# Optimization experiments

Measured on AMD Instinct MI355X. Metric: run time of the kernel, lower is better.

The kernel has to match this reference:

```python
import jax, jax.numpy as jnp
import numpy as np

EPS = 1e-12  # torch F.normalize default eps


def setup_inputs() -> dict:
    key = jax.random.key(0)
    k1, k2, k3, k4 = jax.random.split(key, 4)
    dim, heads, b, h, w = 192, 6, 2, 48, 48
    scale = 1.0 / np.sqrt(dim)
    return {
        "inp": jax.random.normal(k1, (b, dim, h, w), dtype=jnp.float32),
        "wq": jax.random.normal(k2, (dim, dim), dtype=jnp.float32) * scale,
        "wk": jax.random.normal(k3, (dim, dim), dtype=jnp.float32) * scale,
        "wv": jax.random.normal(k4, (dim, dim), dtype=jnp.float32) * scale,
        "temperature": jnp.ones((heads, 1, 1), dtype=jnp.float32),
    }


def _l2norm_lastdim(x):
    # torch F.normalize(x, dim=-1): x / max(||x||_2, eps)
    n = jnp.sqrt(jnp.sum(x * x, axis=-1, keepdims=True))
    return x / jnp.maximum(n, EPS)


def reference(inp, wq, wk, wv, temperature):
    b, c, h, w = inp.shape
    heads = temperature.shape[0]
    ch = c // heads
    n = h * w
    x = inp.reshape(b, c, n)  # 1x1 conv == channel matmul
    q = jnp.einsum("oc,bcn->bon", wq, x).reshape(b, heads, ch, n)
    k = jnp.einsum("oc,bcn->bon", wk, x).reshape(b, heads, ch, n)
    v = jnp.einsum("oc,bcn->bon", wv, x).reshape(b, heads, ch, n)
    q = _l2norm_lastdim(q)
    k = _l2norm_lastdim(k)
    # k^T @ q over channel dim -> [b, heads, n, n]; temperature [heads,1,1] broadcasts
    attn = jnp.einsum("bhcn,bhcm->bhnm", k, q) * temperature
    attn = jax.nn.softmax(attn, axis=-1)
    return attn, v
```

## Files before the change

### kernel.cpp

```cpp
#include <hip/hip_runtime.h>
#include <hip/hip_bf16.h>
#include <cstdint>

#define NSP   2304
#define NT    144
#define ATTN_ELEMS 63700992

typedef __attribute__((ext_vector_type(8))) __bf16 bf16x8;
typedef __attribute__((ext_vector_type(4))) float  float4v;

__device__ __forceinline__ unsigned short f2bf(float f) {
  union { float f; unsigned int u; } v; v.f = f;
  unsigned int u = v.u;
  unsigned int r = u + 0x7FFFu + ((u >> 16) & 1u);
  return (unsigned short)(r >> 16);
}

__global__ __launch_bounds__(256) void prep_pack(
    const float* __restrict__ wq, const float* __restrict__ wk,
    const float* __restrict__ wv, const float* __restrict__ x,
    unsigned short* __restrict__ Wp, unsigned short* __restrict__ Xp)
{
  int t = blockIdx.x * 256 + threadIdx.x;
  int lane = t & 63;
  int g = t >> 6;
  int quad = lane >> 4, col = lane & 15;
  union { int4 v; unsigned short u[8]; } o;
  if (g < 216) {
    int mt = g / 6, kc = g % 6;
    int oo = mt * 16 + col;
    int c0 = kc * 32 + quad * 8;
    const float* w = (oo < 192) ? (wq + (size_t)oo * 192)
                   : (oo < 384) ? (wk + (size_t)(oo - 192) * 192)
                                : (wv + (size_t)(oo - 384) * 192);
#pragma unroll
    for (int jj = 0; jj < 8; ++jj) o.u[jj] = f2bf(w[c0 + jj]);
    ((int4*)Wp)[(size_t)g * 64 + lane] = o.v;
  } else {
    int gx = g - 216;
    int kc = gx % 6;
    int bnt = gx / 6;
    int b = bnt / 144;
    int n = (bnt % 144) * 16 + col;
    int c0 = kc * 32 + quad * 8;
    const float* xp = x + ((size_t)b * 192 + c0) * NSP + n;
#pragma unroll
    for (int jj = 0; jj < 8; ++jj) o.u[jj] = f2bf(xp[(size_t)jj * NSP]);
    ((int4*)Xp)[(size_t)gx * 64 + lane] = o.v;
  }
}

__global__ __launch_bounds__(256) void proj_mfma(
    const bf16x8* __restrict__ Wp, const bf16x8* __restrict__ Xp,
    float* __restrict__ qws, float* __restrict__ kws, float* __restrict__ vout)
{
  int lane = threadIdx.x & 63, w = threadIdx.x >> 6;
  int ng = blockIdx.x * 4 + w;
  int mt = blockIdx.y;
  int b  = blockIdx.z;
  int nt0 = ng * 4;
  float4v acc0 = {0.f,0.f,0.f,0.f};
  float4v acc1 = acc0, acc2 = acc0, acc3 = acc0;
#pragma unroll
  for (int kc = 0; kc < 6; ++kc) {
    bf16x8 a = Wp[(size_t)(mt * 6 + kc) * 64 + lane];
    const bf16x8* xb = Xp + (size_t)((b * 144 + nt0) * 6 + kc) * 64 + lane;
    acc0 = __builtin_amdgcn_mfma_f32_16x16x32_bf16(a, xb[0],    acc0, 0, 0, 0);
    acc1 = __builtin_amdgcn_mfma_f32_16x16x32_bf16(a, xb[384],  acc1, 0, 0, 0);
    acc2 = __builtin_amdgcn_mfma_f32_16x16x32_bf16(a, xb[768],  acc2, 0, 0, 0);
    acc3 = __builtin_amdgcn_mfma_f32_16x16x32_bf16(a, xb[1152], acc3, 0, 0, 0);
  }
  int quad = lane >> 4, col = lane & 15;
  int o0 = mt * 16 + quad * 4;
  float* dst;
  if (mt < 12)      dst = qws + ((size_t)b * 192 + o0) * NSP;
  else if (mt < 24) dst = kws + ((size_t)b * 192 + (o0 - 192)) * NSP;
  else              dst = vout + ((size_t)b * 192 + (o0 - 384)) * NSP;
  float4v acc[4] = {acc0, acc1, acc2, acc3};
#pragma unroll
  for (int tt = 0; tt < 4; ++tt)
#pragma unroll
    for (int r = 0; r < 4; ++r)
      dst[(size_t)r * NSP + (nt0 + tt) * 16 + col] = acc[tt][r];
}

__global__ __launch_bounds__(256) void rownorm(
    const float* __restrict__ qws, const float* __restrict__ kws,
    float* __restrict__ inv)
{
  int r = blockIdx.x;
  const float* src = (r < 384) ? (qws + (size_t)r * NSP)
                               : (kws + (size_t)(r - 384) * NSP);
  float s = 0.f;
#pragma unroll
  for (int i = 0; i < 9; ++i) { float v = src[threadIdx.x + 256 * i]; s += v * v; }
#pragma unroll
  for (int off = 32; off > 0; off >>= 1) s += __shfl_down(s, off);
  __shared__ float ls[4];
  if ((threadIdx.x & 63) == 0) ls[threadIdx.x >> 6] = s;
  __syncthreads();
  if (threadIdx.x == 0) {
    float tot = ls[0] + ls[1] + ls[2] + ls[3];
    inv[r] = 1.0f / fmaxf(sqrtf(tot), 1e-12f);
  }
}

__global__ __launch_bounds__(256) void packqk(
    const float* __restrict__ qws, const float* __restrict__ kws,
    const float* __restrict__ inv, const float* __restrict__ temp,
    unsigned short* __restrict__ Qp, unsigned short* __restrict__ Kp)
{
  int which = blockIdx.z;
  int bh = blockIdx.y;
  int nc = blockIdx.x;
  const float* src = which ? kws : qws;
  const float* ivp = inv + which * 384;
  int b = bh / 6, h = bh % 6;
  float tmul = which ? temp[h] : 1.0f;
  __shared__ float xs[32][65];
  int t = threadIdx.x;
  const float* base = src + ((size_t)b * 192 + h * 32) * NSP + nc * 64;
#pragma unroll
  for (int i = 0; i < 8; ++i) {
    int idx = t + 256 * i;
    int ch = idx >> 6, nl = idx & 63;
    xs[ch][nl] = base[(size_t)ch * NSP + nl] * (ivp[b * 192 + h * 32 + ch] * tmul);
  }
  __syncthreads();
  int jl = t >> 6, lane = t & 63, quad = lane >> 4, col = lane & 15;
  int jt = nc * 4 + jl;
  union { int4 v; unsigned short u[8]; } o;
#pragma unroll
  for (int jj = 0; jj < 8; ++jj) o.u[jj] = f2bf(xs[quad * 8 + jj][jl * 16 + col]);
  int4* dst = (int4*)(which ? Kp : Qp);
  dst[(size_t)(bh * 144 + jt) * 64 + lane] = o.v;
}

__global__ __launch_bounds__(256) void attn_kernel(
    const bf16x8* __restrict__ Qp, const bf16x8* __restrict__ Kp,
    float* __restrict__ out)
{
  int lane = threadIdx.x & 63, w = threadIdx.x >> 6;
  int itile = blockIdx.x;
  int bh = blockIdx.y;
  bf16x8 kf = Kp[((size_t)bh * NT + itile) * 64 + lane];
  const bf16x8* qb = Qp + (size_t)bh * NT * 64 + lane;
  int jt0 = w * 36;
  float l0 = 0.f, l1 = 0.f, l2 = 0.f, l3 = 0.f;
  for (int jt = jt0; jt < jt0 + 36; ++jt) {
    bf16x8 qf = qb[(size_t)jt * 64];
    float4v acc = {0.f,0.f,0.f,0.f};
    acc = __builtin_amdgcn_mfma_f32_16x16x32_bf16(qf, kf, acc, 0, 0, 0);
    l0 += __expf(acc[0]);
    l1 += __expf(acc[1]);
    l2 += __expf(acc[2]);
    l3 += __expf(acc[3]);
  }
  float lsum = (l0 + l1) + (l2 + l3);
  lsum += __shfl_xor(lsum, 16);
  lsum += __shfl_xor(lsum, 32);
  __shared__ float ls[4][16];
  if (lane < 16) ls[w][lane] = lsum;
  __syncthreads();
  int quad = lane >> 4, col = lane & 15;
  float invl = 1.0f / (ls[0][col] + ls[1][col] + ls[2][col] + ls[3][col]);
  float* ob = out + (size_t)bh * NSP * NSP
                  + (size_t)(itile * 16 + col) * NSP + quad * 4;
  for (int jt = jt0; jt < jt0 + 36; ++jt) {
    bf16x8 qf = qb[(size_t)jt * 64];
    float4v acc = {0.f,0.f,0.f,0.f};
    acc = __builtin_amdgcn_mfma_f32_16x16x32_bf16(qf, kf, acc, 0, 0, 0);
    float4 o;
    o.x = __expf(acc[0]) * invl;
    o.y = __expf(acc[1]) * invl;
    o.z = __expf(acc[2]) * invl;
    o.w = __expf(acc[3]) * invl;
    *(float4*)(ob + (size_t)jt * 16) = o;
  }
}

extern "C" void kernel_launch(void* const* d_in, const int* in_sizes, int n_in,
                              void* d_out, int out_size, void* d_ws, size_t ws_size,
                              hipStream_t stream) {
  const float* x    = (const float*)d_in[0];
  const float* wq   = (const float*)d_in[1];
  const float* wk   = (const float*)d_in[2];
  const float* wv   = (const float*)d_in[3];
  const float* temp = (const float*)d_in[4];

  float* attn_out = (float*)d_out;
  float* vout     = attn_out + (size_t)ATTN_ELEMS;

  float* qws = (float*)d_ws;
  float* kws = qws + 884736;
  float* inv = kws + 884736;
  unsigned short* Wp = (unsigned short*)(inv + 768);
  unsigned short* Xp = Wp + 110592;
  unsigned short* Qp = Xp + 884736;
  unsigned short* Kp = Qp + 884736;

  hipLaunchKernelGGL(prep_pack, dim3(486), dim3(256), 0, stream,
                     wq, wk, wv, x, Wp, Xp);
  hipLaunchKernelGGL(proj_mfma, dim3(9, 36, 2), dim3(256), 0, stream,
                     (const bf16x8*)Wp, (const bf16x8*)Xp, qws, kws, vout);
  hipLaunchKernelGGL(rownorm, dim3(768), dim3(256), 0, stream, qws, kws, inv);
  hipLaunchKernelGGL(packqk, dim3(36, 12, 2), dim3(256), 0, stream,
                     qws, kws, inv, temp, Qp, Kp);
  hipLaunchKernelGGL(attn_kernel, dim3(144, 12), dim3(256), 0, stream,
                     (const bf16x8*)Qp, (const bf16x8*)Kp, attn_out);
}
```

Before: 296.9 us.

## Stage softmax exponentials in LDS, fuse row norms into projection, coalesce stores

The attention kernel now writes its first-pass exponentials as bf16 into a padded LDS tile. The normalize-and-store pass reads that tile and writes full contiguous rows with nontemporal float4 stores, instead of recomputing the MFMA and exp and writing 64-byte strided fragments. The separate rownorm kernel is removed: sums of squares are reduced in proj_mfma and accumulated with atomics, and packqk computes the inverse norm itself. V outputs also use nontemporal stores. The change trades about 74 KB of LDS per block (lower occupancy) and bf16 rounding of the exponentials for fewer launches and better-coalesced writes of the dominant output.

```diff
diff --git a/kernel.cpp b/kernel.cpp
--- a/kernel.cpp
+++ b/kernel.cpp
@@ -5,6 +5,8 @@
 #define NSP   2304
 #define NT    144
 #define ATTN_ELEMS 63700992
+#define EPAD  2312
+#define ATTN_LDS (16*EPAD*2 + 64*4 + 16*4)
 
 typedef __attribute__((ext_vector_type(8))) __bf16 bf16x8;
 typedef __attribute__((ext_vector_type(4))) float  float4v;
@@ -19,8 +21,13 @@
 __global__ __launch_bounds__(256) void prep_pack(
     const float* __restrict__ wq, const float* __restrict__ wk,
     const float* __restrict__ wv, const float* __restrict__ x,
-    unsigned short* __restrict__ Wp, unsigned short* __restrict__ Xp)
-{
+    unsigned short* __restrict__ Wp, unsigned short* __restrict__ Xp,
+    float* __restrict__ sumsq)
+{
+  if (blockIdx.x < 3) {
+    int z = blockIdx.x * 256 + threadIdx.x;
+    if (z < 768) sumsq[z] = 0.0f;
+  }
   int t = blockIdx.x * 256 + threadIdx.x;
   int lane = t & 63;
   int g = t >> 6;
@@ -52,7 +59,8 @@
 
 __global__ __launch_bounds__(256) void proj_mfma(
     const bf16x8* __restrict__ Wp, const bf16x8* __restrict__ Xp,
-    float* __restrict__ qws, float* __restrict__ kws, float* __restrict__ vout)
+    float* __restrict__ qws, float* __restrict__ kws, float* __restrict__ vout,
+    float* __restrict__ sumsq)
 {
   int lane = threadIdx.x & 63, w = threadIdx.x >> 6;
   int ng = blockIdx.x * 4 + w;
@@ -72,49 +80,49 @@
   }
   int quad = lane >> 4, col = lane & 15;
   int o0 = mt * 16 + quad * 4;
+  float4v acc[4] = {acc0, acc1, acc2, acc3};
+  bool isv = (mt >= 24);
   float* dst;
   if (mt < 12)      dst = qws + ((size_t)b * 192 + o0) * NSP;
   else if (mt < 24) dst = kws + ((size_t)b * 192 + (o0 - 192)) * NSP;
   else              dst = vout + ((size_t)b * 192 + (o0 - 384)) * NSP;
-  float4v acc[4] = {acc0, acc1, acc2, acc3};
 #pragma unroll
   for (int tt = 0; tt < 4; ++tt)
 #pragma unroll
+    for (int r = 0; r < 4; ++r) {
+      float* p = dst + (size_t)r * NSP + (nt0 + tt) * 16 + col;
+      if (isv) __builtin_nontemporal_store(acc[tt][r], p);
+      else     *p = acc[tt][r];
+    }
+  if (!isv) {
+    float s[4];
+#pragma unroll
     for (int r = 0; r < 4; ++r)
-      dst[(size_t)r * NSP + (nt0 + tt) * 16 + col] = acc[tt][r];
-}
-
-__global__ __launch_bounds__(256) void rownorm(
-    const float* __restrict__ qws, const float* __restrict__ kws,
-    float* __restrict__ inv)
-{
-  int r = blockIdx.x;
-  const float* src = (r < 384) ? (qws + (size_t)r * NSP)
-                               : (kws + (size_t)(r - 384) * NSP);
-  float s = 0.f;
-#pragma unroll
-  for (int i = 0; i < 9; ++i) { float v = src[threadIdx.x + 256 * i]; s += v * v; }
-#pragma unroll
-  for (int off = 32; off > 0; off >>= 1) s += __shfl_down(s, off);
-  __shared__ float ls[4];
-  if ((threadIdx.x & 63) == 0) ls[threadIdx.x >> 6] = s;
-  __syncthreads();
-  if (threadIdx.x == 0) {
-    float tot = ls[0] + ls[1] + ls[2] + ls[3];
-    inv[r] = 1.0f / fmaxf(sqrtf(tot), 1e-12f);
+      s[r] = acc0[r]*acc0[r] + acc1[r]*acc1[r] + acc2[r]*acc2[r] + acc3[r]*acc3[r];
+#pragma unroll
+    for (int off = 1; off < 16; off <<= 1)
+#pragma unroll
+      for (int r = 0; r < 4; ++r) s[r] += __shfl_xor(s[r], off);
+    if (col == 0) {
+      int base = (mt < 12) ? (b * 192 + mt * 16)
+                           : (384 + b * 192 + (mt - 12) * 16);
+#pragma unroll
+      for (int r = 0; r < 4; ++r)
+        atomicAdd(&sumsq[base + quad * 4 + r], s[r]);
+    }
   }
 }
 
 __global__ __launch_bounds__(256) void packqk(
     const float* __restrict__ qws, const float* __restrict__ kws,
-    const float* __restrict__ inv, const float* __restrict__ temp,
+    const float* __restrict__ sumsq, const float* __restrict__ temp,
     unsigned short* __restrict__ Qp, unsigned short* __restrict__ Kp)
 {
   int which = blockIdx.z;
   int bh = blockIdx.y;
   int nc = blockIdx.x;
   const float* src = which ? kws : qws;
-  const float* ivp = inv + which * 384;
+  const float* ssp = sumsq + which * 384;
   int b = bh / 6, h = bh % 6;
   float tmul = which ? temp[h] : 1.0f;
   __shared__ float xs[32][65];
@@ -124,7 +132,9 @@
   for (int i = 0; i < 8; ++i) {
     int idx = t + 256 * i;
     int ch = idx >> 6, nl = idx & 63;
-    xs[ch][nl] = base[(size_t)ch * NSP + nl] * (ivp[b * 192 + h * 32 + ch] * tmul);
+    float ss = ssp[b * 192 + h * 32 + ch];
+    float iv = tmul / fmaxf(sqrtf(ss), 1e-12f);
+    xs[ch][nl] = base[(size_t)ch * NSP + nl] * iv;
   }
   __syncthreads();
   int jl = t >> 6, lane = t & 63, quad = lane >> 4, col = lane & 15;
@@ -140,42 +150,53 @@
     const bf16x8* __restrict__ Qp, const bf16x8* __restrict__ Kp,
     float* __restrict__ out)
 {
-  int lane = threadIdx.x & 63, w = threadIdx.x >> 6;
+  extern __shared__ char smem[];
+  unsigned short* eS = (unsigned short*)smem;
+  float* ls   = (float*)(smem + 16 * EPAD * 2);
+  float* invf = ls + 64;
+  int t = threadIdx.x;
+  int lane = t & 63, w = t >> 6;
   int itile = blockIdx.x;
   int bh = blockIdx.y;
   bf16x8 kf = Kp[((size_t)bh * NT + itile) * 64 + lane];
   const bf16x8* qb = Qp + (size_t)bh * NT * 64 + lane;
+  int quad = lane >> 4, col = lane & 15;
   int jt0 = w * 36;
   float l0 = 0.f, l1 = 0.f, l2 = 0.f, l3 = 0.f;
+  unsigned short* ewp = eS + col * EPAD + quad * 4;
   for (int jt = jt0; jt < jt0 + 36; ++jt) {
     bf16x8 qf = qb[(size_t)jt * 64];
     float4v acc = {0.f,0.f,0.f,0.f};
     acc = __builtin_amdgcn_mfma_f32_16x16x32_bf16(qf, kf, acc, 0, 0, 0);
-    l0 += __expf(acc[0]);
-    l1 += __expf(acc[1]);
-    l2 += __expf(acc[2]);
-    l3 += __expf(acc[3]);
+    float e0 = __expf(acc[0]), e1 = __expf(acc[1]);
+    float e2 = __expf(acc[2]), e3 = __expf(acc[3]);
+    l0 += e0; l1 += e1; l2 += e2; l3 += e3;
+    union { uint2 v; unsigned short u[4]; } pk;
+    pk.u[0] = f2bf(e0); pk.u[1] = f2bf(e1);
+    pk.u[2] = f2bf(e2); pk.u[3] = f2bf(e3);
+    *(uint2*)(ewp + jt * 16) = pk.v;
   }
   float lsum = (l0 + l1) + (l2 + l3);
   lsum += __shfl_xor(lsum, 16);
   lsum += __shfl_xor(lsum, 32);
-  __shared__ float ls[4][16];
-  if (lane < 16) ls[w][lane] = lsum;
+  if (lane < 16) ls[w * 16 + lane] = lsum;
   __syncthreads();
-  int quad = lane >> 4, col = lane & 15;
-  float invl = 1.0f / (ls[0][col] + ls[1][col] + ls[2][col] + ls[3][col]);
-  float* ob = out + (size_t)bh * NSP * NSP
-                  + (size_t)(itile * 16 + col) * NSP + quad * 4;
-  for (int jt = jt0; jt < jt0 + 36; ++jt) {
-    bf16x8 qf = qb[(size_t)jt * 64];
-    float4v acc = {0.f,0.f,0.f,0.f};
-    acc = __builtin_amdgcn_mfma_f32_16x16x32_bf16(qf, kf, acc, 0, 0, 0);
-    float4 o;
-    o.x = __expf(acc[0]) * invl;
-    o.y = __expf(acc[1]) * invl;
-    o.z = __expf(acc[2]) * invl;
-    o.w = __expf(acc[3]) * invl;
-    *(float4*)(ob + (size_t)jt * 16) = o;
+  if (t < 16) invf[t] = 1.0f / (ls[t] + ls[16 + t] + ls[32 + t] + ls[48 + t]);
+  __syncthreads();
+  float* obase = out + (size_t)bh * NSP * NSP + (size_t)(itile * 16) * NSP;
+#pragma unroll 4
+  for (int it = 0; it < 36; ++it) {
+    int c = it * 256 + t;
+    int i = c / 576;
+    int j4 = c - i * 576;
+    float iv = invf[i];
+    uint2 pk = *(const uint2*)(eS + i * EPAD + j4 * 4);
+    float4v o;
+    o.x = __uint_as_float(pk.x << 16) * iv;
+    o.y = __uint_as_float(pk.x & 0xffff0000u) * iv;
+    o.z = __uint_as_float(pk.y << 16) * iv;
+    o.w = __uint_as_float(pk.y & 0xffff0000u) * iv;
+    __builtin_nontemporal_store(o, (float4v*)(obase + (size_t)i * NSP + j4 * 4));
   }
 }
 
@@ -193,19 +214,25 @@
 
   float* qws = (float*)d_ws;
   float* kws = qws + 884736;
-  float* inv = kws + 884736;
-  unsigned short* Wp = (unsigned short*)(inv + 768);
+  float* sumsq = kws + 884736;
+  unsigned short* Wp = (unsigned short*)(sumsq + 768);
   unsigned short* Xp = Wp + 110592;
   unsigned short* Qp = Xp + 884736;
   unsigned short* Kp = Qp + 884736;
 
+  static bool attr_set = false;
+  if (!attr_set) {
+    (void)hipFuncSetAttribute((const void*)attn_kernel,
+                        hipFuncAttributeMaxDynamicSharedMemorySize, ATTN_LDS);
+    attr_set = true;
+  }
+
   hipLaunchKernelGGL(prep_pack, dim3(486), dim3(256), 0, stream,
-                     wq, wk, wv, x, Wp, Xp);
+                     wq, wk, wv, x, Wp, Xp, sumsq);
   hipLaunchKernelGGL(proj_mfma, dim3(9, 36, 2), dim3(256), 0, stream,
-                     (const bf16x8*)Wp, (const bf16x8*)Xp, qws, kws, vout);
-  hipLaunchKernelGGL(rownorm, dim3(768), dim3(256), 0, stream, qws, kws, inv);
+                     (const bf16x8*)Wp, (const bf16x8*)Xp, qws, kws, vout, sumsq);
   hipLaunchKernelGGL(packqk, dim3(36, 12, 2), dim3(256), 0, stream,
-                     qws, kws, inv, temp, Qp, Kp);
-  hipLaunchKernelGGL(attn_kernel, dim3(144, 12), dim3(256), 0, stream,
+                     qws, kws, sumsq, temp, Qp, Kp);
+  hipLaunchKernelGGL(attn_kernel, dim3(144, 12), dim3(256), ATTN_LDS, stream,
                      (const bf16x8*)Qp, (const bf16x8*)Kp, attn_out);
 }
```

New measurement: 299.7 us. No clear change (+0.9%).
